# Optimization experiments

Measured on AMD Instinct MI355X. Metric: run time of the kernel, lower is better.

## Reference

```python
import jax, jax.numpy as jnp
import numpy as np

D, B, L, E, H, F = 6, 4, 2048, 1024, 16, 4096
DH = E // H
DECAY = 16.0
CSCALE = 1.0
EPS = 1e-5


def _ln(x, w, b):
    m = jnp.mean(x, axis=-1, keepdims=True)
    v = jnp.mean(jnp.square(x - m), axis=-1, keepdims=True)
    return (x - m) * jax.lax.rsqrt(v + EPS) * w + b


def setup_inputs() -> dict:
    key = jax.random.key(0)
    ks = jax.random.split(key, 10)
    s = 0.02
    f32 = jnp.float32
    return {
        "x": jax.random.normal(ks[0], (B, L, E), f32),
        "Wq": jax.random.normal(ks[1], (D, E, E), f32) * s,
        "Wk": jax.random.normal(ks[2], (D, E, E), f32) * s,
        "bq": jnp.zeros((D, E), f32),
        "bk": jnp.zeros((D, E), f32),
        "ln1_w": jnp.ones((D, E), f32), "ln1_b": jnp.zeros((D, E), f32),
        "ln2_w": jnp.ones((D, E), f32), "ln2_b": jnp.zeros((D, E), f32),
        "ln3_w": jnp.ones((D, E), f32), "ln3_b": jnp.zeros((D, E), f32),
        "W1": jax.random.normal(ks[3], (D, F, E), f32) * s,
        "b1": jnp.zeros((D, F), f32),
        "W2": jax.random.normal(ks[4], (D, E, F), f32) * s,
        "b2": jnp.zeros((D, E), f32),
    }


def reference(x, Wq, Wk, bq, bk, ln1_w, ln1_b, ln2_w, ln2_b, ln3_w, ln3_b, W1, b1, W2, b2):
    seq = x.shape[1]
    pos = jnp.arange(seq)
    # exponential relative-position bias exp(-|i-j|/decay), shared by all layers
    rel = jnp.exp(-jnp.abs(pos[:, None] - pos[None, :]).astype(x.dtype) / DECAY)
    inv_sqrt_d = 1.0 / np.sqrt(DH)

    def layer(h, p):
        (wq, wk, bq_, bk_, l1w, l1b, l2w, l2b, l3w, l3b, w1, b1_, w2, b2_) = p
        bh, sl, _ = h.shape
        q = (h @ wq.T + bq_).reshape(bh, sl, H, DH)
        k = (h @ wk.T + bk_).reshape(bh, sl, H, DH)
        scores = jnp.einsum('blhd,bmhd->bhlm', q, k) * inv_sqrt_d
        # torch MHA need_weights=True averages softmax weights over heads
        w_avg = jax.nn.softmax(scores, axis=-1).mean(axis=1)  # [B,L,L]
        new_w = jax.nn.softmax(CSCALE * w_avg + rel[None], axis=-1)
        sa = jnp.einsum('blm,bme->ble', new_w, h)  # value = raw residual stream
        h1 = _ln(h + sa, l1w, l1b)
        h2 = _ln(h1, l2w, l2b)  # Noop cross-attn block (LayerNorm scale-invariant)
        ff = jax.nn.relu(h2 @ w1.T + b1_) @ w2.T + b2_
        return _ln(h2 + ff, l3w, l3b), None

    out, _ = jax.lax.scan(layer, x, (Wq, Wk, bq, bk, ln1_w, ln1_b, ln2_w, ln2_b,
                                     ln3_w, ln3_b, W1, b1, W2, b2))
    return out
```

## Files before the change

### kernel.cpp

```cpp
#include <hip/hip_runtime.h>

#define D_ 6
#define B_ 4
#define L_ 2048
#define E_ 1024
#define H_ 16
#define F_ 4096
#define BL_ (B_ * L_)
#define QKS 2048
#define EPS_ 1e-5f

typedef __bf16 bf16x8 __attribute__((ext_vector_type(8)));
typedef __bf16 bf16x4 __attribute__((ext_vector_type(4)));
typedef float f32x4 __attribute__((ext_vector_type(4)));

__device__ __forceinline__ void gload_lds16(const void* g, void* l) {
  __builtin_amdgcn_global_load_lds(
      (const __attribute__((address_space(1))) void*)g,
      (__attribute__((address_space(3))) void*)l, 16, 0, 0);
}

#define LDA_SUB(P, MH)                                                        \
  _Pragma("unroll") for (int mi = 0; mi < 4; ++mi)                            \
  _Pragma("unroll") for (int kk = 0; kk < 2; ++kk) {                          \
    int r_ = wr + (MH) * 64 + mi * 16 + l15;                                  \
    int cu_ = kk * 4 + l4;                                                    \
    aF[mi][kk] = *(const bf16x8*)&lds[P][0][(r_ * 8 + (cu_ ^ (r_ & 7))) * 8]; \
  }

#define LDB_SUB(P, BF, NH)                                                    \
  _Pragma("unroll") for (int ni = 0; ni < 2; ++ni)                            \
  _Pragma("unroll") for (int kk = 0; kk < 2; ++kk) {                          \
    int r_ = wc + (NH) * 32 + ni * 16 + l15;                                  \
    int cu_ = kk * 4 + l4;                                                    \
    BF[ni][kk] = *(const bf16x8*)&lds[P][1][(r_ * 8 + (cu_ ^ (r_ & 7))) * 8]; \
  }

#define MFMA_Q(AF, BF, MH, NH)                                                \
  _Pragma("unroll") for (int mi = 0; mi < 4; ++mi)                            \
  _Pragma("unroll") for (int ni = 0; ni < 2; ++ni)                            \
  _Pragma("unroll") for (int kk = 0; kk < 2; ++kk)                            \
    acc[(MH) * 4 + mi][(NH) * 2 + ni] =                                       \
        __builtin_amdgcn_mfma_f32_16x16x32_bf16(                              \
            AF[mi][kk], BF[ni][kk], acc[(MH) * 4 + mi][(NH) * 2 + ni], 0, 0, 0);

#define PHASE_PRE()                                                           \
  __builtin_amdgcn_s_barrier();                                               \
  asm volatile("s_waitcnt lgkmcnt(0)" ::: "memory");                          \
  __builtin_amdgcn_sched_barrier(0);                                          \
  __builtin_amdgcn_s_setprio(1)

#define PHASE_POST()                                                          \
  __builtin_amdgcn_s_setprio(0);                                              \
  __builtin_amdgcn_sched_barrier(0);                                          \
  __builtin_amdgcn_s_barrier()

template <int EPI>
__global__ __launch_bounds__(512, 2) void gemm8p(
    const __bf16* __restrict__ A, const __bf16* __restrict__ Bm,
    float* __restrict__ Cf, __bf16* __restrict__ Cb,
    const float* __restrict__ bias, int M, int N, int K, int lda, int ldb,
    int zk, long strA, long strB, long strC, long strCk) {
  __shared__ __bf16 lds[2][2][256 * 64];
  const int tid = threadIdx.x;
  const int wave = tid >> 6, lane = tid & 63;
  const int l15 = lane & 15, l4 = lane >> 4;
  const int z = blockIdx.y;
  const int kc = (zk == 2) ? (z & 1) : 0;
  const int bat = (zk == 2) ? (z >> 1) : z;
  const __bf16* Ab = A + (long)bat * strA + (long)kc * K;
  const __bf16* Bb = Bm + (long)bat * strB + (long)kc * K;
  const long coff = (long)bat * strC + (long)kc * strCk;

  const int nbx = N >> 8;
  const int nwg = (M >> 8) * nbx;
  const int orig = blockIdx.x;
  const int qq = nwg >> 3, rr = nwg & 7;
  const int xcd = orig & 7, lid = orig >> 3;
  const int wg = (xcd < rr ? xcd * (qq + 1) : rr * (qq + 1) + (xcd - rr) * qq) + lid;
  const int row0 = (wg / nbx) * 256, col0 = (wg % nbx) * 256;
  const int wr = (wave >> 2) * 128;
  const int wc = (wave & 3) * 64;

  auto STAGE = [&](int bufi, int mat, int hf, const __bf16* Gp, int ldm,
                   int grow0, int k0) {
#pragma unroll
    for (int j = 0; j < 2; ++j) {
      int rowh = j * 64 + (tid >> 3);
      int row = hf * 128 + rowh;
      const __bf16* src =
          Gp + (long)(grow0 + row) * ldm + k0 + (((lane & 7) ^ (lane >> 3)) << 3);
      __bf16* dst = &lds[bufi][mat][(hf * 1024 + j * 512 + wave * 64) * 8];
      gload_lds16(src, dst);
    }
  };

  const int NT = K >> 6;
  STAGE(0, 0, 0, Ab, lda, row0, 0);
  STAGE(0, 0, 1, Ab, lda, row0, 0);
  STAGE(0, 1, 0, Bb, ldb, col0, 0);
  STAGE(0, 1, 1, Bb, ldb, col0, 0);
  STAGE(1, 0, 0, Ab, lda, row0, 64);
  STAGE(1, 1, 0, Bb, ldb, col0, 64);
  STAGE(1, 0, 1, Ab, lda, row0, 64);
  asm volatile("s_waitcnt vmcnt(6)" ::: "memory");
  __builtin_amdgcn_s_barrier();

  f32x4 acc[8][4];
#pragma unroll
  for (int i = 0; i < 8; ++i)
#pragma unroll
    for (int j = 0; j < 4; ++j) acc[i][j] = (f32x4){0.f, 0.f, 0.f, 0.f};
  bf16x8 aF[4][2], b0F[2][2], b1F[2][2];

  for (int t = 0; t < NT; ++t) {
    const int p = t & 1;
    const int kA = (t + 1 < NT ? t + 1 : NT - 1) << 6;
    const int kB = (t + 2 < NT ? t + 2 : NT - 1) << 6;
    LDA_SUB(p, 0);
    LDB_SUB(p, b0F, 0);
    STAGE(p ^ 1, 1, 1, Bb, ldb, col0, kA);
    PHASE_PRE();
    MFMA_Q(aF, b0F, 0, 0);
    PHASE_POST();
    LDB_SUB(p, b1F, 1);
    PHASE_PRE();
    MFMA_Q(aF, b1F, 0, 1);
    PHASE_POST();
    LDA_SUB(p, 1);
    STAGE(p, 1, 0, Bb, ldb, col0, kB);
    PHASE_PRE();
    MFMA_Q(aF, b0F, 1, 0);
    PHASE_POST();
    STAGE(p, 0, 0, Ab, lda, row0, kB);
    STAGE(p, 0, 1, Ab, lda, row0, kB);
    __builtin_amdgcn_s_barrier();
    __builtin_amdgcn_sched_barrier(0);
    __builtin_amdgcn_s_setprio(1);
    MFMA_Q(aF, b1F, 1, 1);
    __builtin_amdgcn_s_setprio(0);
    __builtin_amdgcn_sched_barrier(0);
    asm volatile("s_waitcnt vmcnt(6)" ::: "memory");
    __builtin_amdgcn_s_barrier();
  }
  asm volatile("s_waitcnt vmcnt(0)" ::: "memory");

#pragma unroll
  for (int i = 0; i < 8; ++i) {
    int row = row0 + wr + (i >> 2) * 64 + (i & 3) * 16 + l4 * 4;
#pragma unroll
    for (int j = 0; j < 4; ++j) {
      int col = col0 + wc + (j >> 1) * 32 + (j & 1) * 16 + l15;
      float bval = 0.f;
      if constexpr (EPI == 1 || EPI == 2) bval = bias[col];
#pragma unroll
      for (int r = 0; r < 4; ++r) {
        long crow = row + r;
        float v = acc[i][j][r];
        if constexpr (EPI == 1 || EPI == 2) v += bval;
        if constexpr (EPI == 2) v = fmaxf(v, 0.f);
        long ci = coff + crow * N + col;
        if constexpr (EPI == 1 || EPI == 2)
          Cb[ci] = (__bf16)v;
        else
          Cf[ci] = v;
      }
    }
  }
}

__global__ __launch_bounds__(256, 2) void attn_stats_kernel(
    const __bf16* __restrict__ qk, float* __restrict__ sinv) {
  __shared__ __bf16 sQ[64 * 72];
  __shared__ __bf16 sK[64 * 72];
  const int tid = threadIdx.x, wave = tid >> 6, lane = tid & 63;
  const int l15 = lane & 15, l4 = lane >> 4;
  const int l0 = blockIdx.x * 64, h = blockIdx.y, b = blockIdx.z;

  const __bf16* Qb = qk + ((long)(b * L_ + l0)) * QKS + h * 64;
#pragma unroll
  for (int r = 0; r < 2; ++r) {
    int c = tid + 256 * r;
    int rw = c >> 3, c8 = (c & 7) * 8;
    *(bf16x8*)&sQ[rw * 72 + c8] = *(const bf16x8*)&Qb[(long)rw * QKS + c8];
  }
  __syncthreads();
  bf16x8 aF0 = *(const bf16x8*)&sQ[(wave * 16 + l15) * 72 + l4 * 8];
  bf16x8 aF1 = *(const bf16x8*)&sQ[(wave * 16 + l15) * 72 + 32 + l4 * 8];

  float msum[4];
#pragma unroll
  for (int r = 0; r < 4; ++r) msum[r] = 0.f;

  for (int m0 = 0; m0 < L_; m0 += 64) {
    __syncthreads();
    const __bf16* Kb = qk + ((long)(b * L_ + m0)) * QKS + 1024 + h * 64;
#pragma unroll
    for (int r = 0; r < 2; ++r) {
      int c = tid + 256 * r;
      int rw = c >> 3, c8 = (c & 7) * 8;
      *(bf16x8*)&sK[rw * 72 + c8] = *(const bf16x8*)&Kb[(long)rw * QKS + c8];
    }
    __syncthreads();
#pragma unroll
    for (int ni = 0; ni < 4; ++ni) {
      bf16x8 b0 = *(const bf16x8*)&sK[(ni * 16 + l15) * 72 + l4 * 8];
      bf16x8 b1 = *(const bf16x8*)&sK[(ni * 16 + l15) * 72 + 32 + l4 * 8];
      f32x4 s = (f32x4){0.f, 0.f, 0.f, 0.f};
      s = __builtin_amdgcn_mfma_f32_16x16x32_bf16(aF0, b0, s, 0, 0, 0);
      s = __builtin_amdgcn_mfma_f32_16x16x32_bf16(aF1, b1, s, 0, 0, 0);
#pragma unroll
      for (int r = 0; r < 4; ++r) msum[r] += __expf(s[r] * 0.125f);
    }
  }
#pragma unroll
  for (int r = 0; r < 4; ++r) {
    float s = msum[r];
    for (int d = 1; d < 16; d <<= 1) s += __shfl_xor(s, d, 64);
    if (l15 == 0) {
      long idx = ((long)(b * H_ + h)) * L_ + l0 + wave * 16 + l4 * 4 + r;
      sinv[idx] = 1.0f / s;
    }
  }
}

__global__ __launch_bounds__(256, 2) void attn_probs_kernel(
    const __bf16* __restrict__ qk, const float* __restrict__ sinv,
    __bf16* __restrict__ P) {
  __shared__ __bf16 sQ[64 * 72];
  __shared__ __bf16 sK[64 * 72];
  const int tid = threadIdx.x, wave = tid >> 6, lane = tid & 63;
  const int l15 = lane & 15, l4 = lane >> 4;
  const int m0 = blockIdx.x * 64, l0 = blockIdx.y * 64, b = blockIdx.z;

  float wacc[4][4];
#pragma unroll
  for (int i = 0; i < 4; ++i)
#pragma unroll
    for (int j = 0; j < 4; ++j) wacc[i][j] = 0.f;

  for (int h = 0; h < H_; ++h) {
    __syncthreads();
#pragma unroll
    for (int r = 0; r < 2; ++r) {
      int c = tid + 256 * r;
      int rw = c >> 3, c8 = (c & 7) * 8;
      *(bf16x8*)&sQ[rw * 72 + c8] =
          *(const bf16x8*)&qk[((long)(b * L_ + l0 + rw)) * QKS + h * 64 + c8];
      *(bf16x8*)&sK[rw * 72 + c8] =
          *(const bf16x8*)&qk[((long)(b * L_ + m0 + rw)) * QKS + 1024 + h * 64 + c8];
    }
    __syncthreads();
    bf16x8 aF0 = *(const bf16x8*)&sQ[(wave * 16 + l15) * 72 + l4 * 8];
    bf16x8 aF1 = *(const bf16x8*)&sQ[(wave * 16 + l15) * 72 + 32 + l4 * 8];
    float iv[4];
#pragma unroll
    for (int r = 0; r < 4; ++r) {
      long idx = ((long)(b * H_ + h)) * L_ + l0 + wave * 16 + l4 * 4 + r;
      iv[r] = sinv[idx];
    }
#pragma unroll
    for (int ni = 0; ni < 4; ++ni) {
      bf16x8 b0 = *(const bf16x8*)&sK[(ni * 16 + l15) * 72 + l4 * 8];
      bf16x8 b1 = *(const bf16x8*)&sK[(ni * 16 + l15) * 72 + 32 + l4 * 8];
      f32x4 s = (f32x4){0.f, 0.f, 0.f, 0.f};
      s = __builtin_amdgcn_mfma_f32_16x16x32_bf16(aF0, b0, s, 0, 0, 0);
      s = __builtin_amdgcn_mfma_f32_16x16x32_bf16(aF1, b1, s, 0, 0, 0);
#pragma unroll
      for (int r = 0; r < 4; ++r)
        wacc[ni][r] += __expf(s[r] * 0.125f) * iv[r];
    }
  }
#pragma unroll
  for (int ni = 0; ni < 4; ++ni) {
#pragma unroll
    for (int r = 0; r < 4; ++r) {
      int row = l0 + wave * 16 + l4 * 4 + r;
      int col = m0 + ni * 16 + l15;
      float rel = __expf(-fabsf((float)(row - col)) * (1.0f / 16.0f));
      float t = wacc[ni][r] * (1.0f / H_) + rel;
      P[((long)b * L_ + row) * L_ + col] = (__bf16)__expf(t);
    }
  }
}

__global__ __launch_bounds__(256, 4) void rowinv_kernel(
    const __bf16* __restrict__ P, float* __restrict__ rowinv) {
  const long row = blockIdx.x;
  const __bf16* p = P + row * (long)L_;
  bf16x8 v = *(const bf16x8*)&p[threadIdx.x * 8];
  float s = 0.f;
#pragma unroll
  for (int j = 0; j < 8; ++j) s += (float)v[j];
  for (int d = 1; d < 64; d <<= 1) s += __shfl_xor(s, d, 64);
  __shared__ float sh[4];
  if ((threadIdx.x & 63) == 0) sh[threadIdx.x >> 6] = s;
  __syncthreads();
  if (threadIdx.x == 0) rowinv[row] = 1.0f / (sh[0] + sh[1] + sh[2] + sh[3]);
}

__device__ __forceinline__ void wave_reduce2(float& a, float& b) {
#pragma unroll
  for (int d = 1; d < 64; d <<= 1) {
    a += __shfl_xor(a, d, 64);
    b += __shfl_xor(b, d, 64);
  }
}

__global__ __launch_bounds__(256, 4) void ln12_kernel(
    const float* __restrict__ hin, const float* __restrict__ p0,
    const float* __restrict__ p1, const float* __restrict__ rowinv,
    const float* __restrict__ w1, const float* __restrict__ b1,
    const float* __restrict__ w2, const float* __restrict__ b2,
    float* __restrict__ h2f, __bf16* __restrict__ h2b) {
  __shared__ float sh[8];
  const int tid = threadIdx.x;
  const long row = blockIdx.x;
  const long base = row * E_ + tid * 4;
  const float rinv = rowinv[row];
  f32x4 hv = *(const f32x4*)&hin[base];
  f32x4 p0v = *(const f32x4*)&p0[base];
  f32x4 p1v = *(const f32x4*)&p1[base];
  float y[4];
  float s1 = 0.f, s2 = 0.f;
#pragma unroll
  for (int j = 0; j < 4; ++j) {
    y[j] = hv[j] + rinv * (p0v[j] + p1v[j]);
    s1 += y[j];
    s2 += y[j] * y[j];
  }
  wave_reduce2(s1, s2);
  if ((tid & 63) == 0) { sh[(tid >> 6) * 2] = s1; sh[(tid >> 6) * 2 + 1] = s2; }
  __syncthreads();
  s1 = sh[0] + sh[2] + sh[4] + sh[6];
  s2 = sh[1] + sh[3] + sh[5] + sh[7];
  float mean = s1 * (1.f / E_);
  float var = s2 * (1.f / E_) - mean * mean;
  float rs = rsqrtf(var + EPS_);
  f32x4 wv = *(const f32x4*)&w1[tid * 4];
  f32x4 bv = *(const f32x4*)&b1[tid * 4];
  float h1[4];
  s1 = 0.f; s2 = 0.f;
#pragma unroll
  for (int j = 0; j < 4; ++j) {
    h1[j] = (y[j] - mean) * rs * wv[j] + bv[j];
    s1 += h1[j];
    s2 += h1[j] * h1[j];
  }
  __syncthreads();
  wave_reduce2(s1, s2);
  if ((tid & 63) == 0) { sh[(tid >> 6) * 2] = s1; sh[(tid >> 6) * 2 + 1] = s2; }
  __syncthreads();
  s1 = sh[0] + sh[2] + sh[4] + sh[6];
  s2 = sh[1] + sh[3] + sh[5] + sh[7];
  mean = s1 * (1.f / E_);
  var = s2 * (1.f / E_) - mean * mean;
  rs = rsqrtf(var + EPS_);
  wv = *(const f32x4*)&w2[tid * 4];
  bv = *(const f32x4*)&b2[tid * 4];
  f32x4 o;
  bf16x4 ob;
#pragma unroll
  for (int j = 0; j < 4; ++j) {
    float v = (h1[j] - mean) * rs * wv[j] + bv[j];
    o[j] = v;
    ob[j] = (__bf16)v;
  }
  *(f32x4*)&h2f[base] = o;
  *(bf16x4*)&h2b[base] = ob;
}

__global__ __launch_bounds__(256, 4) void ln3_kernel(
    const float* __restrict__ h2f, const float* __restrict__ p0,
    const float* __restrict__ p1, const float* __restrict__ bias2,
    const float* __restrict__ w3, const float* __restrict__ b3,
    float* __restrict__ outf, __bf16* __restrict__ outb) {
  __shared__ float sh[8];
  const int tid = threadIdx.x;
  const long row = blockIdx.x;
  const long base = row * E_ + tid * 4;
  f32x4 hv = *(const f32x4*)&h2f[base];
  f32x4 p0v = *(const f32x4*)&p0[base];
  f32x4 p1v = *(const f32x4*)&p1[base];
  f32x4 b2v = *(const f32x4*)&bias2[tid * 4];
  float y[4];
  float s1 = 0.f, s2 = 0.f;
#pragma unroll
  for (int j = 0; j < 4; ++j) {
    y[j] = hv[j] + p0v[j] + p1v[j] + b2v[j];
    s1 += y[j];
    s2 += y[j] * y[j];
  }
  wave_reduce2(s1, s2);
  if ((tid & 63) == 0) { sh[(tid >> 6) * 2] = s1; sh[(tid >> 6) * 2 + 1] = s2; }
  __syncthreads();
  s1 = sh[0] + sh[2] + sh[4] + sh[6];
  s2 = sh[1] + sh[3] + sh[5] + sh[7];
  float mean = s1 * (1.f / E_);
  float var = s2 * (1.f / E_) - mean * mean;
  float rs = rsqrtf(var + EPS_);
  f32x4 wv = *(const f32x4*)&w3[tid * 4];
  f32x4 bv = *(const f32x4*)&b3[tid * 4];
  f32x4 o;
  bf16x4 ob;
#pragma unroll
  for (int j = 0; j < 4; ++j) {
    float v = (y[j] - mean) * rs * wv[j] + bv[j];
    o[j] = v;
    ob[j] = (__bf16)v;
  }
  *(f32x4*)&outf[base] = o;
  *(bf16x4*)&outb[base] = ob;
}

__global__ __launch_bounds__(256, 4) void transpose_kernel(
    const __bf16* __restrict__ X, __bf16* __restrict__ XT) {
  __shared__ __bf16 t[64 * 72];
  const int l0 = blockIdx.x * 64, e0 = blockIdx.y * 64, b = blockIdx.z;
  const int tid = threadIdx.x;
#pragma unroll
  for (int r = 0; r < 2; ++r) {
    int c = tid + 256 * r;
    int rw = c >> 3, c8 = (c & 7) * 8;
    *(bf16x8*)&t[rw * 72 + c8] =
        *(const bf16x8*)&X[((long)(b * L_) + l0 + rw) * E_ + e0 + c8];
  }
  __syncthreads();
#pragma unroll
  for (int r = 0; r < 2; ++r) {
    int c = tid + 256 * r;
    int er = c >> 3, l8 = (c & 7) * 8;
    bf16x8 v;
#pragma unroll
    for (int j = 0; j < 8; ++j) v[j] = t[(l8 + j) * 72 + er];
    *(bf16x8*)&XT[((long)(b * E_) + e0 + er) * L_ + l0 + l8] = v;
  }
}

__global__ __launch_bounds__(256, 4) void f32_to_bf16_kernel(
    const float* __restrict__ x, __bf16* __restrict__ y) {
  long i = ((long)blockIdx.x * 256 + threadIdx.x) * 4;
  f32x4 v = *(const f32x4*)&x[i];
  bf16x4 o;
#pragma unroll
  for (int j = 0; j < 4; ++j) o[j] = (__bf16)v[j];
  *(bf16x4*)&y[i] = o;
}

__global__ __launch_bounds__(256, 4) void build_wqk_kernel(
    const float* __restrict__ Wq, const float* __restrict__ Wk,
    __bf16* __restrict__ out) {
  long i = ((long)blockIdx.x * 256 + threadIdx.x) * 4;
  long d = i >> 21;
  long rem = i & ((1L << 21) - 1);
  long row = rem >> 10, col = rem & 1023;
  const float* src = (row < 1024)
                         ? &Wq[(d << 20) + (row << 10) + col]
                         : &Wk[(d << 20) + ((row - 1024) << 10) + col];
  f32x4 v = *(const f32x4*)src;
  bf16x4 o;
#pragma unroll
  for (int j = 0; j < 4; ++j) o[j] = (__bf16)v[j];
  *(bf16x4*)&out[i] = o;
}

__global__ __launch_bounds__(256, 4) void build_bqk_kernel(
    const float* __restrict__ bq, const float* __restrict__ bk,
    float* __restrict__ out) {
  int i = blockIdx.x * 256 + threadIdx.x;
  int d = i >> 11, c = i & 2047;
  out[i] = (c < 1024) ? bq[d * 1024 + c] : bk[d * 1024 + c - 1024];
}

extern "C" void kernel_launch(void* const* d_in, const int* in_sizes, int n_in,
                              void* d_out, int out_size, void* d_ws,
                              size_t ws_size, hipStream_t stream) {
  const float* x = (const float*)d_in[0];
  const float* Wq = (const float*)d_in[1];
  const float* Wk = (const float*)d_in[2];
  const float* bq = (const float*)d_in[3];
  const float* bk = (const float*)d_in[4];
  const float* l1w = (const float*)d_in[5];
  const float* l1b = (const float*)d_in[6];
  const float* l2w = (const float*)d_in[7];
  const float* l2b = (const float*)d_in[8];
  const float* l3w = (const float*)d_in[9];
  const float* l3b = (const float*)d_in[10];
  const float* W1 = (const float*)d_in[11];
  const float* b1 = (const float*)d_in[12];
  const float* W2 = (const float*)d_in[13];
  const float* b2 = (const float*)d_in[14];

  char* p = (char*)d_ws;
  auto take = [&](size_t bytes) -> char* {
    char* r = p;
    p += (bytes + 255) & ~(size_t)255;
    return r;
  };
  __bf16* wqk_bf = (__bf16*)take((size_t)D_ * 2048 * 1024 * 2);
  __bf16* w1_bf = (__bf16*)take((size_t)D_ * F_ * E_ * 2);
  __bf16* w2_bf = (__bf16*)take((size_t)D_ * E_ * F_ * 2);
  __bf16* h_bf = (__bf16*)take((size_t)BL_ * E_ * 2);
  __bf16* hT = (__bf16*)take((size_t)BL_ * E_ * 2);
  __bf16* qk_bf = (__bf16*)take((size_t)BL_ * QKS * 2);
  __bf16* Pbuf = (__bf16*)take((size_t)B_ * L_ * L_ * 2);
  __bf16* ffmid = qk_bf;
  float* bqk = (float*)take((size_t)D_ * 2048 * 4);
  float* sinv = (float*)take((size_t)B_ * H_ * L_ * 4);
  float* rowinv = (float*)take((size_t)B_ * L_ * 4);
  float* part = (float*)take((size_t)2 * BL_ * E_ * 4);
  float* part0 = part;
  float* part1 = part + (size_t)BL_ * E_;
  float* hbuf = (float*)take((size_t)BL_ * E_ * 4);

  build_wqk_kernel<<<D_ * 2048 * 1024 / 1024, 256, 0, stream>>>(Wq, Wk, wqk_bf);
  build_bqk_kernel<<<D_ * 2048 / 256, 256, 0, stream>>>(bq, bk, bqk);
  f32_to_bf16_kernel<<<D_ * F_ * E_ / 1024, 256, 0, stream>>>(W1, w1_bf);
  f32_to_bf16_kernel<<<D_ * E_ * F_ / 1024, 256, 0, stream>>>(W2, w2_bf);
  f32_to_bf16_kernel<<<BL_ * E_ / 1024, 256, 0, stream>>>(x, h_bf);
  transpose_kernel<<<dim3(L_ / 64, E_ / 64, B_), 256, 0, stream>>>(h_bf, hT);

  const float* h_in = x;
  for (int d = 0; d < D_; ++d) {
    gemm8p<1><<<dim3(256, 1), 512, 0, stream>>>(
        h_bf, wqk_bf + (size_t)d * 2048 * 1024, nullptr, qk_bf,
        bqk + d * 2048, BL_, 2048, E_, E_, E_, 1, 0, 0, 0, 0);
    attn_stats_kernel<<<dim3(L_ / 64, H_, B_), 256, 0, stream>>>(qk_bf, sinv);
    attn_probs_kernel<<<dim3(L_ / 64, L_ / 64, B_), 256, 0, stream>>>(
        qk_bf, sinv, Pbuf);
    rowinv_kernel<<<B_ * L_, 256, 0, stream>>>(Pbuf, rowinv);
    gemm8p<0><<<dim3(32, 8), 512, 0, stream>>>(
        Pbuf, hT, part, nullptr, nullptr, L_, E_, L_ / 2, L_, L_, 2,
        (long)L_ * L_, (long)E_ * L_, (long)L_ * E_, (long)BL_ * E_);
    ln12_kernel<<<BL_, 256, 0, stream>>>(h_in, part0, part1, rowinv,
                                         l1w + d * E_, l1b + d * E_,
                                         l2w + d * E_, l2b + d * E_, hbuf,
                                         h_bf);
    gemm8p<2><<<dim3(512, 1), 512, 0, stream>>>(
        h_bf, w1_bf + (size_t)d * F_ * E_, nullptr, ffmid, b1 + d * F_, BL_,
        F_, E_, E_, E_, 1, 0, 0, 0, 0);
    gemm8p<0><<<dim3(128, 2), 512, 0, stream>>>(
        ffmid, w2_bf + (size_t)d * E_ * F_, part, nullptr, nullptr, BL_, E_,
        F_ / 2, F_, F_, 2, 0, 0, 0, (long)BL_ * E_);
    float* outp = (d == D_ - 1) ? (float*)d_out : hbuf;
    ln3_kernel<<<BL_, 256, 0, stream>>>(hbuf, part0, part1, b2 + d * E_,
                                        l3w + d * E_, l3b + d * E_, outp,
                                        h_bf);
    if (d < D_ - 1) {
      transpose_kernel<<<dim3(L_ / 64, E_ / 64, B_), 256, 0, stream>>>(h_bf, hT);
      h_in = hbuf;
    }
  }
}
```

Measured before the change: 2.551 ms.

## Double-buffer attention Q/K tiles with async global-to-LDS loads and swizzle

The attention stats and probs kernels now stage Q/K tiles through direct global-to-LDS loads into double-buffered, XOR-swizzled shared memory. The next tile is prefetched while MFMAs run on the current one, and explicit vmcnt waits plus barriers replace the old synchronous load/sync loop. The aim is to hide global load latency and remove the register round-trip. Separately, the transpose kernel's LDS row padding shrinks from 72 to 66 elements to change the bank-conflict pattern. That padding leaves the 16-byte vector stores misaligned for odd rows.

```diff
diff --git a/kernel.cpp b/kernel.cpp
--- a/kernel.cpp
+++ b/kernel.cpp
@@ -19,6 +19,21 @@
       (const __attribute__((address_space(1))) void*)g,
       (__attribute__((address_space(3))) void*)l, 16, 0, 0);
 }
+
+__device__ __forceinline__ void stage_tile64(__bf16* ldsb,
+                                             const __bf16* gbase, long ldg,
+                                             int tid) {
+#pragma unroll
+  for (int j = 0; j < 2; ++j) {
+    int unit = j * 256 + tid;
+    int row = unit >> 3, cu = unit & 7;
+    const __bf16* src = gbase + (long)row * ldg + ((cu ^ (row & 7)) << 3);
+    gload_lds16(src, ldsb + (long)((j * 256 + (tid & ~63)) << 3));
+  }
+}
+
+#define RD_FRAG(ldsb, r_, kk) \
+  (*(const bf16x8*)&(ldsb)[((r_) * 8 + (((kk) * 4 + l4) ^ ((r_) & 7))) * 8])
 
 #define LDA_SUB(P, MH)                                                        \
   _Pragma("unroll") for (int mi = 0; mi < 4; ++mi)                            \
@@ -171,47 +186,44 @@
 
 __global__ __launch_bounds__(256, 2) void attn_stats_kernel(
     const __bf16* __restrict__ qk, float* __restrict__ sinv) {
-  __shared__ __bf16 sQ[64 * 72];
-  __shared__ __bf16 sK[64 * 72];
+  __shared__ __bf16 sQ[64 * 64];
+  __shared__ __bf16 sK[2][64 * 64];
   const int tid = threadIdx.x, wave = tid >> 6, lane = tid & 63;
   const int l15 = lane & 15, l4 = lane >> 4;
   const int l0 = blockIdx.x * 64, h = blockIdx.y, b = blockIdx.z;
-
   const __bf16* Qb = qk + ((long)(b * L_ + l0)) * QKS + h * 64;
-#pragma unroll
-  for (int r = 0; r < 2; ++r) {
-    int c = tid + 256 * r;
-    int rw = c >> 3, c8 = (c & 7) * 8;
-    *(bf16x8*)&sQ[rw * 72 + c8] = *(const bf16x8*)&Qb[(long)rw * QKS + c8];
-  }
-  __syncthreads();
-  bf16x8 aF0 = *(const bf16x8*)&sQ[(wave * 16 + l15) * 72 + l4 * 8];
-  bf16x8 aF1 = *(const bf16x8*)&sQ[(wave * 16 + l15) * 72 + 32 + l4 * 8];
-
-  float msum[4];
-#pragma unroll
-  for (int r = 0; r < 4; ++r) msum[r] = 0.f;
-
-  for (int m0 = 0; m0 < L_; m0 += 64) {
-    __syncthreads();
-    const __bf16* Kb = qk + ((long)(b * L_ + m0)) * QKS + 1024 + h * 64;
-#pragma unroll
-    for (int r = 0; r < 2; ++r) {
-      int c = tid + 256 * r;
-      int rw = c >> 3, c8 = (c & 7) * 8;
-      *(bf16x8*)&sK[rw * 72 + c8] = *(const bf16x8*)&Kb[(long)rw * QKS + c8];
-    }
-    __syncthreads();
+  const __bf16* Kb = qk + ((long)b * L_) * QKS + 1024 + h * 64;
+
+  stage_tile64(sQ, Qb, QKS, tid);
+  stage_tile64(sK[0], Kb, QKS, tid);
+  asm volatile("s_waitcnt vmcnt(0)" ::: "memory");
+  __builtin_amdgcn_s_barrier();
+
+  const int rA = wave * 16 + l15;
+  const bf16x8 aF0 = RD_FRAG(sQ, rA, 0);
+  const bf16x8 aF1 = RD_FRAG(sQ, rA, 1);
+
+  float msum[4] = {0.f, 0.f, 0.f, 0.f};
+  int p = 0;
+  for (int m0 = 0; m0 < 32; ++m0) {
+    const int mn = (m0 + 1 < 32) ? m0 + 1 : 31;
+    stage_tile64(sK[p ^ 1], Kb + (long)mn * 64 * QKS, QKS, tid);
+    asm volatile("s_waitcnt vmcnt(2)" ::: "memory");
+    __builtin_amdgcn_s_barrier();
 #pragma unroll
     for (int ni = 0; ni < 4; ++ni) {
-      bf16x8 b0 = *(const bf16x8*)&sK[(ni * 16 + l15) * 72 + l4 * 8];
-      bf16x8 b1 = *(const bf16x8*)&sK[(ni * 16 + l15) * 72 + 32 + l4 * 8];
+      const int rB = ni * 16 + l15;
+      bf16x8 b0 = RD_FRAG(sK[p], rB, 0);
+      bf16x8 b1 = RD_FRAG(sK[p], rB, 1);
       f32x4 s = (f32x4){0.f, 0.f, 0.f, 0.f};
       s = __builtin_amdgcn_mfma_f32_16x16x32_bf16(aF0, b0, s, 0, 0, 0);
       s = __builtin_amdgcn_mfma_f32_16x16x32_bf16(aF1, b1, s, 0, 0, 0);
 #pragma unroll
       for (int r = 0; r < 4; ++r) msum[r] += __expf(s[r] * 0.125f);
     }
+    asm volatile("" ::: "memory");
+    __builtin_amdgcn_s_barrier();
+    p ^= 1;
   }
 #pragma unroll
   for (int r = 0; r < 4; ++r) {
@@ -227,11 +239,15 @@
 __global__ __launch_bounds__(256, 2) void attn_probs_kernel(
     const __bf16* __restrict__ qk, const float* __restrict__ sinv,
     __bf16* __restrict__ P) {
-  __shared__ __bf16 sQ[64 * 72];
-  __shared__ __bf16 sK[64 * 72];
+  __shared__ __bf16 sT[2][2][64 * 64];
   const int tid = threadIdx.x, wave = tid >> 6, lane = tid & 63;
   const int l15 = lane & 15, l4 = lane >> 4;
   const int m0 = blockIdx.x * 64, l0 = blockIdx.y * 64, b = blockIdx.z;
+  const __bf16* Qb = qk + ((long)(b * L_ + l0)) * QKS;
+  const __bf16* Kb = qk + ((long)(b * L_ + m0)) * QKS + 1024;
+
+  stage_tile64(sT[0][0], Qb, QKS, tid);
+  stage_tile64(sT[0][1], Kb, QKS, tid);
 
   float wacc[4][4];
 #pragma unroll
@@ -239,30 +255,27 @@
 #pragma unroll
     for (int j = 0; j < 4; ++j) wacc[i][j] = 0.f;
 
+  const int rA = wave * 16 + l15;
+  int p = 0;
   for (int h = 0; h < H_; ++h) {
-    __syncthreads();
-#pragma unroll
-    for (int r = 0; r < 2; ++r) {
-      int c = tid + 256 * r;
-      int rw = c >> 3, c8 = (c & 7) * 8;
-      *(bf16x8*)&sQ[rw * 72 + c8] =
-          *(const bf16x8*)&qk[((long)(b * L_ + l0 + rw)) * QKS + h * 64 + c8];
-      *(bf16x8*)&sK[rw * 72 + c8] =
-          *(const bf16x8*)&qk[((long)(b * L_ + m0 + rw)) * QKS + 1024 + h * 64 + c8];
-    }
-    __syncthreads();
-    bf16x8 aF0 = *(const bf16x8*)&sQ[(wave * 16 + l15) * 72 + l4 * 8];
-    bf16x8 aF1 = *(const bf16x8*)&sQ[(wave * 16 + l15) * 72 + 32 + l4 * 8];
+    const int hn = (h + 1 < H_) ? h + 1 : H_ - 1;
+    stage_tile64(sT[p ^ 1][0], Qb + hn * 64, QKS, tid);
+    stage_tile64(sT[p ^ 1][1], Kb + hn * 64, QKS, tid);
     float iv[4];
 #pragma unroll
     for (int r = 0; r < 4; ++r) {
       long idx = ((long)(b * H_ + h)) * L_ + l0 + wave * 16 + l4 * 4 + r;
       iv[r] = sinv[idx];
     }
+    asm volatile("s_waitcnt vmcnt(4)" ::: "memory");
+    __builtin_amdgcn_s_barrier();
+    bf16x8 aF0 = RD_FRAG(sT[p][0], rA, 0);
+    bf16x8 aF1 = RD_FRAG(sT[p][0], rA, 1);
 #pragma unroll
     for (int ni = 0; ni < 4; ++ni) {
-      bf16x8 b0 = *(const bf16x8*)&sK[(ni * 16 + l15) * 72 + l4 * 8];
-      bf16x8 b1 = *(const bf16x8*)&sK[(ni * 16 + l15) * 72 + 32 + l4 * 8];
+      const int rB = ni * 16 + l15;
+      bf16x8 b0 = RD_FRAG(sT[p][1], rB, 0);
+      bf16x8 b1 = RD_FRAG(sT[p][1], rB, 1);
       f32x4 s = (f32x4){0.f, 0.f, 0.f, 0.f};
       s = __builtin_amdgcn_mfma_f32_16x16x32_bf16(aF0, b0, s, 0, 0, 0);
       s = __builtin_amdgcn_mfma_f32_16x16x32_bf16(aF1, b1, s, 0, 0, 0);
@@ -270,6 +283,9 @@
       for (int r = 0; r < 4; ++r)
         wacc[ni][r] += __expf(s[r] * 0.125f) * iv[r];
     }
+    asm volatile("" ::: "memory");
+    __builtin_amdgcn_s_barrier();
+    p ^= 1;
   }
 #pragma unroll
   for (int ni = 0; ni < 4; ++ni) {
@@ -415,14 +431,14 @@
 
 __global__ __launch_bounds__(256, 4) void transpose_kernel(
     const __bf16* __restrict__ X, __bf16* __restrict__ XT) {
-  __shared__ __bf16 t[64 * 72];
+  __shared__ __bf16 t[64 * 66];
   const int l0 = blockIdx.x * 64, e0 = blockIdx.y * 64, b = blockIdx.z;
   const int tid = threadIdx.x;
 #pragma unroll
   for (int r = 0; r < 2; ++r) {
     int c = tid + 256 * r;
     int rw = c >> 3, c8 = (c & 7) * 8;
-    *(bf16x8*)&t[rw * 72 + c8] =
+    *(bf16x8*)&t[rw * 66 + c8] =
         *(const bf16x8*)&X[((long)(b * L_) + l0 + rw) * E_ + e0 + c8];
   }
   __syncthreads();
@@ -432,7 +448,7 @@
     int er = c >> 3, l8 = (c & 7) * 8;
     bf16x8 v;
 #pragma unroll
-    for (int j = 0; j < 8; ++j) v[j] = t[(l8 + j) * 72 + er];
+    for (int j = 0; j < 8; ++j) v[j] = t[(l8 + j) * 66 + er];
     *(bf16x8*)&XT[((long)(b * E_) + e0 + er) * L_ + l0 + l8] = v;
   }
 }
```

Measured after the change: 2.526 ms. Within noise of the previous version (-1.0%).
